# Optimization experiments

Hardware: AMD Instinct MI355X
Metric: run time of the kernel (lower is better)

Reference implementation:

```python
import jax, jax.numpy as jnp
import numpy as np

HIDDEN = 256
NUM_CLASSES = 96
ENC_FEAT = 256


def setup_inputs() -> dict:
    key = jax.random.key(0)
    ks = jax.random.split(key, 12)
    B, T, D, H, C = 1024, 64, ENC_FEAT, HIDDEN, NUM_CLASSES
    s = 0.05
    return {
        "batch_H": jax.random.normal(ks[0], (B, T, D), jnp.float32),
        "text": jax.random.randint(ks[1], (B, 26), 0, C, jnp.int64),
        "batch_max_length": 25,
        # attention cell params
        "Wi2h": jax.random.normal(ks[2], (D, H), jnp.float32) * s,
        "Wh2h": jax.random.normal(ks[3], (H, H), jnp.float32) * s,
        "bh2h": jnp.zeros((H,), jnp.float32),
        "w_score": jax.random.normal(ks[4], (H, 1), jnp.float32) * s,
        # LSTMCell params (keras gate order: i, f, c, o)
        "Wx": jax.random.normal(ks[5], (D + C, 4 * H), jnp.float32) * s,
        "Wh": jax.random.normal(ks[6], (H, 4 * H), jnp.float32) * s,
        "b_lstm": jnp.concatenate([jnp.zeros((H,)), jnp.ones((H,)), jnp.zeros((2 * H,))]).astype(jnp.float32),
        # generator
        "Wg": jax.random.normal(ks[7], (H, C), jnp.float32) * s,
        "bg": jnp.zeros((C,), jnp.float32),
    }


def _decode(batch_H, text, num_steps, Wi2h, Wh2h, bh2h, w_score, Wx, Wh, b_lstm, Wg, bg):
    B = batch_H.shape[0]
    H = Wh.shape[0]
    C = Wg.shape[1]
    # precompute encoder projection once: [B, T, H]
    batch_H_proj = jnp.einsum("btd,dh->bth", batch_H, Wi2h)

    def step(carry, char_idx):
        h, c = carry
        onehot = jax.nn.one_hot(char_idx, C, dtype=batch_H.dtype)  # [B, C]
        # Bahdanau score: tanh(Wi2h*H + Wh2h*h) @ w_score -> [B, T, 1]
        hp = (h @ Wh2h + bh2h)[:, None, :]
        e = jnp.tanh(batch_H_proj + hp) @ w_score
        alpha = jax.nn.softmax(e, axis=1)  # [B, T, 1]
        context = jnp.sum(alpha * batch_H, axis=1)  # [B, D]
        x = jnp.concatenate([context, onehot], axis=1)  # [B, D+C]
        gates = x @ Wx + h @ Wh + b_lstm  # [B, 4H]
        i_g, f_g, g_g, o_g = jnp.split(gates, 4, axis=1)
        c_new = jax.nn.sigmoid(f_g) * c + jax.nn.sigmoid(i_g) * jnp.tanh(g_g)
        h_new = jax.nn.sigmoid(o_g) * jnp.tanh(c_new)
        return (h_new, c_new), h_new

    h0 = jnp.zeros((B, H), batch_H.dtype)
    c0 = jnp.zeros((B, H), batch_H.dtype)
    chars = text[:, :num_steps].T  # [num_steps, B]
    _, hiddens = jax.lax.scan(step, (h0, c0), chars)
    output_hiddens = jnp.transpose(hiddens, (1, 0, 2))  # [B, num_steps, H]
    probs = output_hiddens @ Wg + bg  # [B, num_steps, C]
    return probs


def reference(batch_H, text, batch_max_length, Wi2h, Wh2h, bh2h, w_score, Wx, Wh, b_lstm, Wg, bg):
    num_steps = batch_max_length + 1
    return _decode(batch_H, text, num_steps, Wi2h, Wh2h, bh2h, w_score, Wx, Wh, b_lstm, Wg, bg)
```

## Files before the change

kernel.cpp:

```cpp
#include <hip/hip_runtime.h>

constexpr int B  = 1024;
constexpr int T  = 64;
constexpr int D  = 256;
constexpr int H  = 256;
constexpr int C  = 96;
constexpr int NS = 26;
constexpr int G  = 4 * H;

__device__ __forceinline__ float fsig(float x) {
    return __builtin_amdgcn_rcpf(1.0f + __expf(-x));
}
__device__ __forceinline__ float ftanh(float x) {
    float e = __expf(2.0f * x);
    return fmaf(-2.0f, __builtin_amdgcn_rcpf(e + 1.0f), 1.0f);
}

__global__ __launch_bounds__(256) void proj_kernel(
        const float* __restrict__ bH, const float* __restrict__ Wi2h,
        float* __restrict__ proj) {
    __shared__ float xs[32 * 256];
    const int row0 = blockIdx.x * 32;
    const int tid = threadIdx.x;

    const float4* src = reinterpret_cast<const float4*>(bH + (size_t)row0 * D);
    float4* dst = reinterpret_cast<float4*>(xs);
#pragma unroll
    for (int i = 0; i < 8; ++i) dst[tid + 256 * i] = src[tid + 256 * i];
    __syncthreads();

    const int wv = tid >> 6, lane = tid & 63;
    const int r0 = wv * 8;
    const int c0 = lane * 4;
    float4 acc[8];
#pragma unroll
    for (int r = 0; r < 8; ++r) acc[r] = make_float4(0.f, 0.f, 0.f, 0.f);

    for (int k = 0; k < D; k += 4) {
        const float4 w0 = *reinterpret_cast<const float4*>(&Wi2h[(k + 0) * H + c0]);
        const float4 w1 = *reinterpret_cast<const float4*>(&Wi2h[(k + 1) * H + c0]);
        const float4 w2 = *reinterpret_cast<const float4*>(&Wi2h[(k + 2) * H + c0]);
        const float4 w3 = *reinterpret_cast<const float4*>(&Wi2h[(k + 3) * H + c0]);
#pragma unroll
        for (int r = 0; r < 8; ++r) {
            const float4 x = *reinterpret_cast<const float4*>(&xs[(r0 + r) * 256 + k]);
            acc[r].x = fmaf(x.x, w0.x, fmaf(x.y, w1.x, fmaf(x.z, w2.x, fmaf(x.w, w3.x, acc[r].x))));
            acc[r].y = fmaf(x.x, w0.y, fmaf(x.y, w1.y, fmaf(x.z, w2.y, fmaf(x.w, w3.y, acc[r].y))));
            acc[r].z = fmaf(x.x, w0.z, fmaf(x.y, w1.z, fmaf(x.z, w2.z, fmaf(x.w, w3.z, acc[r].z))));
            acc[r].w = fmaf(x.x, w0.w, fmaf(x.y, w1.w, fmaf(x.z, w2.w, fmaf(x.w, w3.w, acc[r].w))));
        }
    }
#pragma unroll
    for (int r = 0; r < 8; ++r)
        *reinterpret_cast<float4*>(&proj[(size_t)(row0 + r0 + r) * H + c0]) = acc[r];
}

__global__ __launch_bounds__(512) void decoder_kernel(
        const float* __restrict__ proj, const float* __restrict__ bH,
        const int* __restrict__ text, const float* __restrict__ Wx,
        const float* __restrict__ Wh, const float* __restrict__ b_lstm,
        const float* __restrict__ Wh2h, const float* __restrict__ bh2h,
        const float* __restrict__ w_score, float* __restrict__ hiddens) {
    __shared__ float hp_s[4][256];
    __shared__ float h_s[4][256];
    __shared__ float c_s[4][256];
    __shared__ float ctx_s[4][256];
    __shared__ float gates[4][1024];
    __shared__ float alpha_s[4][64];
    __shared__ float ws_s[256];

    const int row0 = blockIdx.x * 4;
    const int tid = threadIdx.x;
    const int wv = tid >> 6, lane = tid & 63;

    for (int i = tid; i < 1024; i += 512) {
        const int r = i >> 8, j = i & 255;
        h_s[r][j] = 0.0f;
        c_s[r][j] = 0.0f;
        hp_s[r][j] = bh2h[j];
    }
    if (tid < 256) ws_s[tid] = w_score[tid];
    __syncthreads();

    for (int t = 0; t < NS; ++t) {
        if (wv < 4) {
            const int r = wv;
            const float* pb = proj + (size_t)(row0 + r) * T * H;
            const float4 hv = *reinterpret_cast<const float4*>(&hp_s[r][lane * 4]);
            const float4 wq = *reinterpret_cast<const float4*>(&ws_s[lane * 4]);
            for (int tt = 0; tt < T; tt += 4) {
                float s[4];
#pragma unroll
                for (int q = 0; q < 4; ++q) {
                    const float4 p =
                        *reinterpret_cast<const float4*>(&pb[(tt + q) * H + lane * 4]);
                    s[q] = ftanh(p.x + hv.x) * wq.x + ftanh(p.y + hv.y) * wq.y +
                           ftanh(p.z + hv.z) * wq.z + ftanh(p.w + hv.w) * wq.w;
                }
#pragma unroll
                for (int off = 32; off > 0; off >>= 1) {
#pragma unroll
                    for (int q = 0; q < 4; ++q) s[q] += __shfl_xor(s[q], off);
                }
                if (lane == 0) {
#pragma unroll
                    for (int q = 0; q < 4; ++q) alpha_s[r][tt + q] = s[q];
                }
            }
            {
                const float v = alpha_s[r][lane];
                float m = v;
#pragma unroll
                for (int off = 32; off > 0; off >>= 1) m = fmaxf(m, __shfl_xor(m, off));
                const float p = __expf(v - m);
                float sum = p;
#pragma unroll
                for (int off = 32; off > 0; off >>= 1) sum += __shfl_xor(sum, off);
                alpha_s[r][lane] = p * __builtin_amdgcn_rcpf(sum);
            }
            {
                const float* xb = bH + (size_t)(row0 + r) * T * D;
                float4 cacc = make_float4(0.f, 0.f, 0.f, 0.f);
#pragma unroll 4
                for (int tt = 0; tt < T; ++tt) {
                    const float av = alpha_s[r][tt];
                    const float4 x =
                        *reinterpret_cast<const float4*>(&xb[tt * D + lane * 4]);
                    cacc.x = fmaf(av, x.x, cacc.x);
                    cacc.y = fmaf(av, x.y, cacc.y);
                    cacc.z = fmaf(av, x.z, cacc.z);
                    cacc.w = fmaf(av, x.w, cacc.w);
                }
                *reinterpret_cast<float4*>(&ctx_s[r][lane * 4]) = cacc;
            }
        } else {
            const int cw = (wv - 4) * 256 + lane * 4;
            float4 a0, a1, a2, a3;
            {
                const float4 bb = *reinterpret_cast<const float4*>(&b_lstm[cw]);
                const int ch0 = text[(row0 + 0) * NS + t];
                const int ch1 = text[(row0 + 1) * NS + t];
                const int ch2 = text[(row0 + 2) * NS + t];
                const int ch3 = text[(row0 + 3) * NS + t];
                const float4 o0 = *reinterpret_cast<const float4*>(&Wx[(size_t)(D + ch0) * G + cw]);
                const float4 o1 = *reinterpret_cast<const float4*>(&Wx[(size_t)(D + ch1) * G + cw]);
                const float4 o2 = *reinterpret_cast<const float4*>(&Wx[(size_t)(D + ch2) * G + cw]);
                const float4 o3 = *reinterpret_cast<const float4*>(&Wx[(size_t)(D + ch3) * G + cw]);
                a0 = make_float4(bb.x + o0.x, bb.y + o0.y, bb.z + o0.z, bb.w + o0.w);
                a1 = make_float4(bb.x + o1.x, bb.y + o1.y, bb.z + o1.z, bb.w + o1.w);
                a2 = make_float4(bb.x + o2.x, bb.y + o2.y, bb.z + o2.z, bb.w + o2.w);
                a3 = make_float4(bb.x + o3.x, bb.y + o3.y, bb.z + o3.z, bb.w + o3.w);
            }
            for (int k = 0; k < H; k += 4) {
                const float4 w0 = *reinterpret_cast<const float4*>(&Wh[(size_t)(k + 0) * G + cw]);
                const float4 w1 = *reinterpret_cast<const float4*>(&Wh[(size_t)(k + 1) * G + cw]);
                const float4 w2 = *reinterpret_cast<const float4*>(&Wh[(size_t)(k + 2) * G + cw]);
                const float4 w3 = *reinterpret_cast<const float4*>(&Wh[(size_t)(k + 3) * G + cw]);
                const float4 x0 = *reinterpret_cast<const float4*>(&h_s[0][k]);
                const float4 x1 = *reinterpret_cast<const float4*>(&h_s[1][k]);
                const float4 x2 = *reinterpret_cast<const float4*>(&h_s[2][k]);
                const float4 x3 = *reinterpret_cast<const float4*>(&h_s[3][k]);
#define ACC4(A, X)                                                              \
    A.x = fmaf(X.x, w0.x, fmaf(X.y, w1.x, fmaf(X.z, w2.x, fmaf(X.w, w3.x, A.x)))); \
    A.y = fmaf(X.x, w0.y, fmaf(X.y, w1.y, fmaf(X.z, w2.y, fmaf(X.w, w3.y, A.y)))); \
    A.z = fmaf(X.x, w0.z, fmaf(X.y, w1.z, fmaf(X.z, w2.z, fmaf(X.w, w3.z, A.z)))); \
    A.w = fmaf(X.x, w0.w, fmaf(X.y, w1.w, fmaf(X.z, w2.w, fmaf(X.w, w3.w, A.w))))
                ACC4(a0, x0);
                ACC4(a1, x1);
                ACC4(a2, x2);
                ACC4(a3, x3);
#undef ACC4
            }
            *reinterpret_cast<float4*>(&gates[0][cw]) = a0;
            *reinterpret_cast<float4*>(&gates[1][cw]) = a1;
            *reinterpret_cast<float4*>(&gates[2][cw]) = a2;
            *reinterpret_cast<float4*>(&gates[3][cw]) = a3;
        }
        __syncthreads();

        {
            const int cw = wv * 128 + lane * 2;
            float2 a0 = *reinterpret_cast<float2*>(&gates[0][cw]);
            float2 a1 = *reinterpret_cast<float2*>(&gates[1][cw]);
            float2 a2 = *reinterpret_cast<float2*>(&gates[2][cw]);
            float2 a3 = *reinterpret_cast<float2*>(&gates[3][cw]);
            for (int k = 0; k < D; k += 4) {
                const float2 w0 = *reinterpret_cast<const float2*>(&Wx[(size_t)(k + 0) * G + cw]);
                const float2 w1 = *reinterpret_cast<const float2*>(&Wx[(size_t)(k + 1) * G + cw]);
                const float2 w2 = *reinterpret_cast<const float2*>(&Wx[(size_t)(k + 2) * G + cw]);
                const float2 w3 = *reinterpret_cast<const float2*>(&Wx[(size_t)(k + 3) * G + cw]);
                const float4 x0 = *reinterpret_cast<const float4*>(&ctx_s[0][k]);
                const float4 x1 = *reinterpret_cast<const float4*>(&ctx_s[1][k]);
                const float4 x2 = *reinterpret_cast<const float4*>(&ctx_s[2][k]);
                const float4 x3 = *reinterpret_cast<const float4*>(&ctx_s[3][k]);
#define ACC2(A, X)                                                              \
    A.x = fmaf(X.x, w0.x, fmaf(X.y, w1.x, fmaf(X.z, w2.x, fmaf(X.w, w3.x, A.x)))); \
    A.y = fmaf(X.x, w0.y, fmaf(X.y, w1.y, fmaf(X.z, w2.y, fmaf(X.w, w3.y, A.y))))
                ACC2(a0, x0);
                ACC2(a1, x1);
                ACC2(a2, x2);
                ACC2(a3, x3);
#undef ACC2
            }
            *reinterpret_cast<float2*>(&gates[0][cw]) = a0;
            *reinterpret_cast<float2*>(&gates[1][cw]) = a1;
            *reinterpret_cast<float2*>(&gates[2][cw]) = a2;
            *reinterpret_cast<float2*>(&gates[3][cw]) = a3;
        }
        __syncthreads();

#pragma unroll
        for (int pp = 0; pp < 2; ++pp) {
            const int r = (tid >> 8) + pp * 2;
            const int j = tid & 255;
            const float gi = gates[r][j];
            const float gf = gates[r][256 + j];
            const float gc = gates[r][512 + j];
            const float go = gates[r][768 + j];
            const float cv = fsig(gf) * c_s[r][j] + fsig(gi) * ftanh(gc);
            c_s[r][j] = cv;
            const float hvv = fsig(go) * ftanh(cv);
            h_s[r][j] = hvv;
            hiddens[((size_t)(row0 + r) * NS + t) * H + j] = hvv;
        }
        __syncthreads();

        {
            const int j = tid & 255;
            const int rb = (tid >> 8) * 2;
            float acc0 = bh2h[j];
            float acc1 = acc0;
            for (int k = 0; k < H; k += 4) {
                const float w0 = Wh2h[(k + 0) * H + j];
                const float w1 = Wh2h[(k + 1) * H + j];
                const float w2 = Wh2h[(k + 2) * H + j];
                const float w3 = Wh2h[(k + 3) * H + j];
                const float4 xa = *reinterpret_cast<const float4*>(&h_s[rb][k]);
                const float4 xb = *reinterpret_cast<const float4*>(&h_s[rb + 1][k]);
                acc0 = fmaf(xa.x, w0, fmaf(xa.y, w1, fmaf(xa.z, w2, fmaf(xa.w, w3, acc0))));
                acc1 = fmaf(xb.x, w0, fmaf(xb.y, w1, fmaf(xb.z, w2, fmaf(xb.w, w3, acc1))));
            }
            hp_s[rb][j] = acc0;
            hp_s[rb + 1][j] = acc1;
        }
        __syncthreads();
    }
}

__global__ __launch_bounds__(192) void gen_kernel(
        const float* __restrict__ hiddens, const float* __restrict__ Wg,
        const float* __restrict__ bg, float* __restrict__ out) {
    const int row0 = blockIdx.x * 16 + (threadIdx.x / 96) * 8;
    const int cc = threadIdx.x % 96;
    float acc[8];
    const float bias = bg[cc];
#pragma unroll
    for (int r = 0; r < 8; ++r) acc[r] = bias;
    for (int k = 0; k < H; k += 4) {
        const float w0 = Wg[(k + 0) * C + cc];
        const float w1 = Wg[(k + 1) * C + cc];
        const float w2 = Wg[(k + 2) * C + cc];
        const float w3 = Wg[(k + 3) * C + cc];
#pragma unroll
        for (int r = 0; r < 8; ++r) {
            const float4 x = *reinterpret_cast<const float4*>(
                &hiddens[(size_t)(row0 + r) * H + k]);
            acc[r] = fmaf(x.x, w0, acc[r]);
            acc[r] = fmaf(x.y, w1, acc[r]);
            acc[r] = fmaf(x.z, w2, acc[r]);
            acc[r] = fmaf(x.w, w3, acc[r]);
        }
    }
#pragma unroll
    for (int r = 0; r < 8; ++r) out[(size_t)(row0 + r) * C + cc] = acc[r];
}

extern "C" void kernel_launch(void* const* d_in, const int* in_sizes, int n_in,
                              void* d_out, int out_size, void* d_ws, size_t ws_size,
                              hipStream_t stream) {
    const float* batch_H = (const float*)d_in[0];
    const int*   text    = (const int*)d_in[1];
    const float* Wi2h    = (const float*)d_in[3];
    const float* Wh2h    = (const float*)d_in[4];
    const float* bh2h    = (const float*)d_in[5];
    const float* w_score = (const float*)d_in[6];
    const float* Wx      = (const float*)d_in[7];
    const float* Wh      = (const float*)d_in[8];
    const float* b_lstm  = (const float*)d_in[9];
    const float* Wg      = (const float*)d_in[10];
    const float* bg      = (const float*)d_in[11];
    float* out = (float*)d_out;

    float* ws      = (float*)d_ws;
    float* proj    = ws;
    float* hiddens = proj + (size_t)B * T * H;

    proj_kernel<<<B * T / 32, 256, 0, stream>>>(batch_H, Wi2h, proj);
    decoder_kernel<<<B / 4, 512, 0, stream>>>(proj, batch_H, text, Wx, Wh, b_lstm,
                                              Wh2h, bh2h, w_score, hiddens);
    gen_kernel<<<B * NS / 16, 192, 0, stream>>>(hiddens, Wg, bg, out);
}
```

Before: 1.477 ms.

## Store encoder projection and batch_H in bf16 with transposed proj layout

Converts batch_H to bf16 in a new conversion kernel and writes the projected encoder features as bf16 in an H-major tiled layout. The decoder then reads half the bytes per step from these two arrays, which it re-reads on each of the 26 steps. The new layout lets each lane compute one score over all hidden units without cross-lane shuffle reductions. It also adds launch bounds for two blocks per CU. The cost is an extra conversion pass and lower precision in attention scores and context, which risks exceeding the tolerance.

```diff
diff --git a/kernel.cpp b/kernel.cpp
--- a/kernel.cpp
+++ b/kernel.cpp
@@ -1,4 +1,5 @@
 #include <hip/hip_runtime.h>
+#include <hip/hip_bf16.h>
 
 constexpr int B  = 1024;
 constexpr int T  = 64;
@@ -15,10 +16,33 @@
     float e = __expf(2.0f * x);
     return fmaf(-2.0f, __builtin_amdgcn_rcpf(e + 1.0f), 1.0f);
 }
+__device__ __forceinline__ float bf_lo(unsigned int p) {
+    union { unsigned int i; float f; } v;
+    v.i = p << 16;
+    return v.f;
+}
+__device__ __forceinline__ float bf_hi(unsigned int p) {
+    union { unsigned int i; float f; } v;
+    v.i = p & 0xFFFF0000u;
+    return v.f;
+}
+__device__ __forceinline__ unsigned short f2bf(float f) {
+    __hip_bfloat16 h = __float2bfloat16(f);
+    return *reinterpret_cast<unsigned short*>(&h);
+}
+
+__global__ __launch_bounds__(256) void cvt_kernel(
+        const float* __restrict__ in, ushort* __restrict__ out) {
+    const int i = blockIdx.x * 256 + threadIdx.x;
+    const float4 v = reinterpret_cast<const float4*>(in)[i];
+    ushort4 o;
+    o.x = f2bf(v.x); o.y = f2bf(v.y); o.z = f2bf(v.z); o.w = f2bf(v.w);
+    reinterpret_cast<ushort4*>(out)[i] = o;
+}
 
 __global__ __launch_bounds__(256) void proj_kernel(
         const float* __restrict__ bH, const float* __restrict__ Wi2h,
-        float* __restrict__ proj) {
+        ushort* __restrict__ proj) {
     __shared__ float xs[32 * 256];
     const int row0 = blockIdx.x * 32;
     const int tid = threadIdx.x;
@@ -51,12 +75,19 @@
         }
     }
 #pragma unroll
-    for (int r = 0; r < 8; ++r)
-        *reinterpret_cast<float4*>(&proj[(size_t)(row0 + r0 + r) * H + c0]) = acc[r];
-}
-
-__global__ __launch_bounds__(512) void decoder_kernel(
-        const float* __restrict__ proj, const float* __restrict__ bH,
+    for (int r = 0; r < 8; ++r) {
+        const int brow = row0 + r0 + r;
+        const int bb = brow >> 6, tt = brow & 63;
+        ushort4 o;
+        o.x = f2bf(acc[r].x); o.y = f2bf(acc[r].y);
+        o.z = f2bf(acc[r].z); o.w = f2bf(acc[r].w);
+        *reinterpret_cast<ushort4*>(
+            &proj[(size_t)bb * H * T + (c0 >> 3) * (T * 8) + tt * 8 + (c0 & 7)]) = o;
+    }
+}
+
+__global__ __launch_bounds__(512, 2) void decoder_kernel(
+        const ushort* __restrict__ proj, const ushort* __restrict__ bHb,
         const int* __restrict__ text, const float* __restrict__ Wx,
         const float* __restrict__ Wh, const float* __restrict__ b_lstm,
         const float* __restrict__ Wh2h, const float* __restrict__ bh2h,
@@ -85,51 +116,45 @@
     for (int t = 0; t < NS; ++t) {
         if (wv < 4) {
             const int r = wv;
-            const float* pb = proj + (size_t)(row0 + r) * T * H;
-            const float4 hv = *reinterpret_cast<const float4*>(&hp_s[r][lane * 4]);
-            const float4 wq = *reinterpret_cast<const float4*>(&ws_s[lane * 4]);
-            for (int tt = 0; tt < T; tt += 4) {
-                float s[4];
-#pragma unroll
-                for (int q = 0; q < 4; ++q) {
-                    const float4 p =
-                        *reinterpret_cast<const float4*>(&pb[(tt + q) * H + lane * 4]);
-                    s[q] = ftanh(p.x + hv.x) * wq.x + ftanh(p.y + hv.y) * wq.y +
-                           ftanh(p.z + hv.z) * wq.z + ftanh(p.w + hv.w) * wq.w;
-                }
-#pragma unroll
-                for (int off = 32; off > 0; off >>= 1) {
-#pragma unroll
-                    for (int q = 0; q < 4; ++q) s[q] += __shfl_xor(s[q], off);
-                }
-                if (lane == 0) {
-#pragma unroll
-                    for (int q = 0; q < 4; ++q) alpha_s[r][tt + q] = s[q];
-                }
+            const ushort* pb = proj + (size_t)(row0 + r) * H * T + lane * 8;
+            float e = 0.0f;
+#pragma unroll 4
+            for (int h = 0; h < H; h += 8) {
+                const uint4 pv = *reinterpret_cast<const uint4*>(pb + (h >> 3) * (T * 8));
+                const float4 hp0 = *reinterpret_cast<const float4*>(&hp_s[r][h]);
+                const float4 hp1 = *reinterpret_cast<const float4*>(&hp_s[r][h + 4]);
+                const float4 w0 = *reinterpret_cast<const float4*>(&ws_s[h]);
+                const float4 w1 = *reinterpret_cast<const float4*>(&ws_s[h + 4]);
+                e += ftanh(bf_lo(pv.x) + hp0.x) * w0.x;
+                e += ftanh(bf_hi(pv.x) + hp0.y) * w0.y;
+                e += ftanh(bf_lo(pv.y) + hp0.z) * w0.z;
+                e += ftanh(bf_hi(pv.y) + hp0.w) * w0.w;
+                e += ftanh(bf_lo(pv.z) + hp1.x) * w1.x;
+                e += ftanh(bf_hi(pv.z) + hp1.y) * w1.y;
+                e += ftanh(bf_lo(pv.w) + hp1.z) * w1.z;
+                e += ftanh(bf_hi(pv.w) + hp1.w) * w1.w;
             }
             {
-                const float v = alpha_s[r][lane];
-                float m = v;
+                float m = e;
 #pragma unroll
                 for (int off = 32; off > 0; off >>= 1) m = fmaxf(m, __shfl_xor(m, off));
-                const float p = __expf(v - m);
+                const float p = __expf(e - m);
                 float sum = p;
 #pragma unroll
                 for (int off = 32; off > 0; off >>= 1) sum += __shfl_xor(sum, off);
                 alpha_s[r][lane] = p * __builtin_amdgcn_rcpf(sum);
             }
             {
-                const float* xb = bH + (size_t)(row0 + r) * T * D;
+                const ushort* xb = bHb + (size_t)(row0 + r) * T * D + lane * 4;
                 float4 cacc = make_float4(0.f, 0.f, 0.f, 0.f);
-#pragma unroll 4
+#pragma unroll 8
                 for (int tt = 0; tt < T; ++tt) {
+                    const ushort4 x4 = *reinterpret_cast<const ushort4*>(xb + tt * D);
                     const float av = alpha_s[r][tt];
-                    const float4 x =
-                        *reinterpret_cast<const float4*>(&xb[tt * D + lane * 4]);
-                    cacc.x = fmaf(av, x.x, cacc.x);
-                    cacc.y = fmaf(av, x.y, cacc.y);
-                    cacc.z = fmaf(av, x.z, cacc.z);
-                    cacc.w = fmaf(av, x.w, cacc.w);
+                    cacc.x = fmaf(av, bf_lo((unsigned)x4.x), cacc.x);
+                    cacc.y = fmaf(av, bf_lo((unsigned)x4.y), cacc.y);
+                    cacc.z = fmaf(av, bf_lo((unsigned)x4.z), cacc.z);
+                    cacc.w = fmaf(av, bf_lo((unsigned)x4.w), cacc.w);
                 }
                 *reinterpret_cast<float4*>(&ctx_s[r][lane * 4]) = cacc;
             }
@@ -291,12 +316,14 @@
     const float* bg      = (const float*)d_in[11];
     float* out = (float*)d_out;
 
-    float* ws      = (float*)d_ws;
-    float* proj    = ws;
-    float* hiddens = proj + (size_t)B * T * H;
-
-    proj_kernel<<<B * T / 32, 256, 0, stream>>>(batch_H, Wi2h, proj);
-    decoder_kernel<<<B / 4, 512, 0, stream>>>(proj, batch_H, text, Wx, Wh, b_lstm,
+    char* wsb = (char*)d_ws;
+    ushort* proj_bf = (ushort*)wsb;
+    ushort* bH_bf   = (ushort*)(wsb + (size_t)B * T * H * 2);
+    float*  hiddens = (float*)(wsb + (size_t)B * T * H * 2 * 2);
+
+    cvt_kernel<<<B * T * D / 4 / 256, 256, 0, stream>>>(batch_H, bH_bf);
+    proj_kernel<<<B * T / 32, 256, 0, stream>>>(batch_H, Wi2h, proj_bf);
+    decoder_kernel<<<B / 4, 512, 0, stream>>>(proj_bf, bH_bf, text, Wx, Wh, b_lstm,
                                               Wh2h, bh2h, w_score, hiddens);
     gen_kernel<<<B * NS / 16, 192, 0, stream>>>(hiddens, Wg, bg, out);
 }
```

After: 1.406 ms. 1.05x faster.
